# Optimization experiments

Measured on AMD Instinct MI355X. Metric: run time of the kernel, lower is better.

Reference implementation:

```python
import jax, jax.numpy as jnp
import numpy as np

N_USER = 100000
N_ITEM = 150000
N = N_USER + N_ITEM
D = 64            # latdim
NNZ = 1250000     # sparse adjacency nnz
BATCH = 16384     # node_ids batch
NUM_GNN_LAYERS = 2
GD = 16           # gate_dim (mamba d_model)
DSTATE = 8
DCONV = 4
EXPAND = 2
DINNER = GD * EXPAND  # 32
DTRANK = 1            # ceil(GD/16)
TEMP = 0.8            # gate_temp


def setup_inputs() -> dict:
    key = jax.random.key(0)
    ks = jax.random.split(key, 20)
    f32 = jnp.float32
    inp = {}
    inp["user_embedding"] = jax.random.normal(ks[0], (N_USER, D), f32) * 0.02
    inp["item_embedding"] = jax.random.normal(ks[1], (N_ITEM, D), f32) * 0.02
    inp["edge_row"] = jax.random.randint(ks[2], (NNZ,), 0, N, dtype=jnp.int32)
    inp["edge_col"] = jax.random.randint(ks[3], (NNZ,), 0, N, dtype=jnp.int32)
    inp["edge_val"] = jax.random.uniform(ks[4], (NNZ,), f32) * 0.1
    inp["node_ids"] = jax.random.randint(ks[5], (BATCH,), 0, N, dtype=jnp.int32)
    # gate params (torch Linear weight layout: [out, in])
    inp["down_w"] = jax.random.normal(ks[6], (GD, D), f32) * 0.02
    inp["in_proj_w"] = jax.random.normal(ks[7], (2 * DINNER, GD), f32) * 0.05
    inp["conv_w"] = jax.random.normal(ks[8], (DINNER, DCONV), f32) * 0.1
    inp["conv_b"] = jnp.zeros((DINNER,), f32)
    inp["x_proj_w"] = jax.random.normal(ks[9], (DTRANK + 2 * DSTATE, DINNER), f32) * 0.05
    inp["dt_proj_w"] = jax.random.normal(ks[10], (DINNER, DTRANK), f32) * 0.1
    inp["dt_proj_b"] = jax.random.normal(ks[11], (DINNER,), f32) * 0.1
    inp["A_log"] = jnp.log(jnp.broadcast_to(jnp.arange(1, DSTATE + 1, dtype=f32), (DINNER, DSTATE)))
    inp["D_param"] = jnp.ones((DINNER,), f32)
    inp["out_proj_w"] = jax.random.normal(ks[12], (GD, DINNER), f32) * 0.05
    inp["ln_g"] = jnp.ones((GD,), f32)
    inp["ln_b"] = jnp.zeros((GD,), f32)
    inp["to_logit_w"] = jax.random.normal(ks[13], (1, GD), f32) * 0.02
    inp["to_logit_b"] = jnp.zeros((1,), f32)
    return inp


def _mamba(g, in_proj_w, conv_w, conv_b, x_proj_w, dt_proj_w, dt_proj_b, A_log, D_param, out_proj_w):
    # g: [B, L, GD] -- standard Mamba block (selective scan)
    Bsz, L, _ = g.shape
    xz = g @ in_proj_w.T                     # [B,L,2*DINNER]
    x, z = jnp.split(xz, 2, axis=-1)         # each [B,L,DINNER]
    # causal depthwise conv1d along L (padding = DCONV-1, truncated to L)
    xp = jnp.pad(x, ((0, 0), (DCONV - 1, 0), (0, 0)))
    xconv = sum(xp[:, k:k + L, :] * conv_w[:, k] for k in range(DCONV)) + conv_b
    x = jax.nn.silu(xconv)
    dbc = x @ x_proj_w.T                     # [B,L,DTRANK+2*DSTATE]
    dt = dbc[..., :DTRANK]
    Bm = dbc[..., DTRANK:DTRANK + DSTATE]
    Cm = dbc[..., DTRANK + DSTATE:]
    dt = jax.nn.softplus(dt @ dt_proj_w.T + dt_proj_b)   # [B,L,DINNER]
    A = -jnp.exp(A_log)                                   # [DINNER,DSTATE]
    dA = jnp.exp(dt[..., None] * A)                       # [B,L,DINNER,DSTATE]
    dBx = dt[..., None] * Bm[:, :, None, :] * x[..., None]

    def step(h, ins):
        dA_t, dBx_t = ins
        h = dA_t * h + dBx_t
        return h, h

    h0 = jnp.zeros((Bsz, DINNER, DSTATE), x.dtype)
    _, hs = jax.lax.scan(step, h0, (jnp.swapaxes(dA, 0, 1), jnp.swapaxes(dBx, 0, 1)))
    hs = jnp.swapaxes(hs, 0, 1)                           # [B,L,DINNER,DSTATE]
    y = jnp.einsum('blds,bls->bld', hs, Cm) + D_param * x
    y = y * jax.nn.silu(z)
    return y @ out_proj_w.T                               # [B,L,GD]


def reference(user_embedding, item_embedding, edge_val, down_w, in_proj_w, conv_w,
              conv_b, x_proj_w, dt_proj_w, dt_proj_b, A_log, D_param, out_proj_w,
              ln_g, ln_b, to_logit_w, to_logit_b, edge_row, edge_col, node_ids):
    embeds = jnp.concatenate([user_embedding, item_embedding], axis=0)   # [N,D]
    seqs = [embeds[node_ids]]
    for _ in range(NUM_GNN_LAYERS):
        # sparse adjacency aggregation: out[r] += val * embeds[c]
        msg = edge_val[:, None] * embeds[edge_col]                       # [NNZ,D]
        embeds = jax.ops.segment_sum(msg, edge_row, num_segments=N)      # [N,D]
        # F.normalize(p=2, dim=1)
        nrm = jnp.linalg.norm(embeds, axis=1, keepdims=True)
        embeds = embeds / jnp.maximum(nrm, 1e-12)
        seqs.append(embeds[node_ids])
    seq = jnp.stack(seqs, axis=1)                                        # [B,L,D]

    # MambaDepthGating._compute_logits (deg_cond disabled)
    g = seq @ down_w.T                                                   # [B,L,GD]
    y = _mamba(g, in_proj_w, conv_w, conv_b, x_proj_w, dt_proj_w, dt_proj_b,
               A_log, D_param, out_proj_w)
    y = y + g
    mu = y.mean(-1, keepdims=True)
    var = y.var(-1, keepdims=True)
    y = (y - mu) / jnp.sqrt(var + 1e-12) * ln_g + ln_b                   # LN eps=1e-12
    logits = (y @ to_logit_w.T + to_logit_b)[..., 0]                     # [B,L]

    # fuse_from_logits, L=3 > 2 -> softmax path, perturbed=False
    w = jax.nn.softmax(logits / max(TEMP, 1e-6), axis=1)                 # [B,L]
    fused = jnp.sum(seq * w[..., None], axis=1)                          # [B,D]
    return fused
```

## Files before the change

kernel.cpp:

```cpp
#include <hip/hip_runtime.h>
#include <math.h>

#define N_USER 100000
#define N_ITEM 150000
#define NTOT   250000
#define D64    64
#define NNZ    1250000
#define BATCH  16384
#define GD     16
#define DSTATE 8
#define DCONV  4
#define DINNER 32
#define LSEQ   3
#define NBLK1  ((NTOT + 1023) >> 10)

__global__ void mark_nids_kernel(const int* __restrict__ nids,
                                 unsigned char* __restrict__ nidf,
                                 unsigned char* __restrict__ needf) {
    int b = blockIdx.x * 256 + threadIdx.x;
    if (b < BATCH) { int r = nids[b]; nidf[r] = 1; needf[r] = 1; }
}

__global__ void mark_need_kernel(const int* __restrict__ erow,
                                 const int* __restrict__ ecol,
                                 const unsigned char* __restrict__ nidf,
                                 unsigned char* __restrict__ needf) {
    int e = (blockIdx.x * 256 + threadIdx.x) * 4;
    if (e + 4 <= NNZ) {
        int4 r = *(const int4*)(erow + e);
        int4 c = *(const int4*)(ecol + e);
        if (nidf[r.x]) needf[c.x] = 1;
        if (nidf[r.y]) needf[c.y] = 1;
        if (nidf[r.z]) needf[c.z] = 1;
        if (nidf[r.w]) needf[c.w] = 1;
    } else {
        for (; e < NNZ; ++e) if (nidf[erow[e]]) needf[ecol[e]] = 1;
    }
}

__global__ void hist_kernel(const int* __restrict__ erow,
                            const unsigned char* __restrict__ needf,
                            int* __restrict__ cnt) {
    int e = (blockIdx.x * 256 + threadIdx.x) * 4;
    if (e + 4 <= NNZ) {
        int4 r = *(const int4*)(erow + e);
        if (needf[r.x]) atomicAdd(&cnt[r.x], 1);
        if (needf[r.y]) atomicAdd(&cnt[r.y], 1);
        if (needf[r.z]) atomicAdd(&cnt[r.z], 1);
        if (needf[r.w]) atomicAdd(&cnt[r.w], 1);
    } else {
        for (; e < NNZ; ++e) {
            int r = erow[e];
            if (needf[r]) atomicAdd(&cnt[r], 1);
        }
    }
}

__global__ __launch_bounds__(256) void scan1_kernel(const int* __restrict__ cnt,
                                                    const unsigned char* __restrict__ flags,
                                                    int* __restrict__ offs,
                                                    int* __restrict__ fpos,
                                                    int* __restrict__ bsum,
                                                    int* __restrict__ fbsum) {
    __shared__ int lds[256];
    __shared__ int lfs[256];
    int t = threadIdx.x;
    int base = (blockIdx.x << 10) + (t << 2);
    int d0 = (base + 0 < NTOT) ? cnt[base + 0] : 0;
    int d1 = (base + 1 < NTOT) ? cnt[base + 1] : 0;
    int d2 = (base + 2 < NTOT) ? cnt[base + 2] : 0;
    int d3 = (base + 3 < NTOT) ? cnt[base + 3] : 0;
    int f0 = (base + 0 < NTOT) ? (int)flags[base + 0] : 0;
    int f1 = (base + 1 < NTOT) ? (int)flags[base + 1] : 0;
    int f2 = (base + 2 < NTOT) ? (int)flags[base + 2] : 0;
    int f3 = (base + 3 < NTOT) ? (int)flags[base + 3] : 0;
    int s  = d0 + d1 + d2 + d3;
    int fs = f0 + f1 + f2 + f3;
    lds[t] = s; lfs[t] = fs;
    __syncthreads();
    for (int off = 1; off < 256; off <<= 1) {
        int v  = (t >= off) ? lds[t - off] : 0;
        int fv = (t >= off) ? lfs[t - off] : 0;
        __syncthreads();
        lds[t] += v; lfs[t] += fv;
        __syncthreads();
    }
    int excl  = lds[t] - s;
    int fexcl = lfs[t] - fs;
    if (base + 0 < NTOT) { offs[base + 0] = excl;                fpos[base + 0] = fexcl; }
    if (base + 1 < NTOT) { offs[base + 1] = excl + d0;           fpos[base + 1] = fexcl + f0; }
    if (base + 2 < NTOT) { offs[base + 2] = excl + d0 + d1;      fpos[base + 2] = fexcl + f0 + f1; }
    if (base + 3 < NTOT) { offs[base + 3] = excl + d0 + d1 + d2; fpos[base + 3] = fexcl + f0 + f1 + f2; }
    if (t == 255) { bsum[blockIdx.x] = lds[255]; fbsum[blockIdx.x] = lfs[255]; }
}

__global__ __launch_bounds__(256) void scan2_kernel(int* __restrict__ bsum,
                                                    int* __restrict__ fbsum) {
    __shared__ int lds[256];
    __shared__ int lfs[256];
    int t = threadIdx.x;
    int v0 = (t < NBLK1) ? bsum[t] : 0;
    int f0 = (t < NBLK1) ? fbsum[t] : 0;
    lds[t] = v0; lfs[t] = f0;
    __syncthreads();
    for (int off = 1; off < 256; off <<= 1) {
        int v  = (t >= off) ? lds[t - off] : 0;
        int fv = (t >= off) ? lfs[t - off] : 0;
        __syncthreads();
        lds[t] += v; lfs[t] += fv;
        __syncthreads();
    }
    if (t < NBLK1) { bsum[t] = lds[t] - v0; fbsum[t] = lfs[t] - f0; }
}

__global__ void scan3_kernel(int* __restrict__ offs, const int* __restrict__ bsum,
                             const int* __restrict__ cnt,
                             const int* __restrict__ fpos, const int* __restrict__ fbsum,
                             const unsigned char* __restrict__ flags,
                             int* __restrict__ cursor,
                             int* __restrict__ row_list, int* __restrict__ nrows) {
    int i = blockIdx.x * 256 + threadIdx.x;
    if (i >= NTOT) return;
    int v = offs[i] + bsum[i >> 10];
    offs[i] = v;
    cursor[i] = v;
    int fp = fpos[i] + fbsum[i >> 10];
    int fl = flags[i];
    if (fl) row_list[fp] = i;
    if (i == NTOT - 1) {
        offs[NTOT] = v + cnt[i];
        nrows[0] = fp + fl;
    }
}

__global__ void fill_kernel(const int* __restrict__ erow, const int* __restrict__ ecol,
                            const float* __restrict__ eval_,
                            int* __restrict__ cursor,
                            const unsigned char* __restrict__ needf,
                            int2* __restrict__ colval) {
    int e = (blockIdx.x * 256 + threadIdx.x) * 4;
    if (e + 4 <= NNZ) {
        int4   r = *(const int4*)(erow + e);
        int4   c = *(const int4*)(ecol + e);
        float4 v = *(const float4*)(eval_ + e);
        if (needf[r.x]) colval[atomicAdd(&cursor[r.x], 1)] = make_int2(c.x, __float_as_int(v.x));
        if (needf[r.y]) colval[atomicAdd(&cursor[r.y], 1)] = make_int2(c.y, __float_as_int(v.y));
        if (needf[r.z]) colval[atomicAdd(&cursor[r.z], 1)] = make_int2(c.z, __float_as_int(v.z));
        if (needf[r.w]) colval[atomicAdd(&cursor[r.w], 1)] = make_int2(c.w, __float_as_int(v.w));
    } else {
        for (; e < NNZ; ++e) {
            int r = erow[e];
            if (needf[r]) colval[atomicAdd(&cursor[r], 1)] = make_int2(ecol[e], __float_as_int(eval_[e]));
        }
    }
}

__global__ __launch_bounds__(256) void layer1_kernel(const float* __restrict__ user,
                                                     const float* __restrict__ item,
                                                     const int*  __restrict__ nrows,
                                                     const int*  __restrict__ row_list,
                                                     const int*  __restrict__ offs,
                                                     const int2* __restrict__ colval,
                                                     float* __restrict__ dst) {
    const float4* user4 = (const float4*)user;
    const float4* item4 = (const float4*)item;

    int gid    = (blockIdx.x << 4) + (threadIdx.x >> 4);
    int lane16 = threadIdx.x & 15;
    if (gid >= nrows[0]) return;
    int row = row_list[gid];
    int o0 = offs[row], o1 = offs[row + 1];

    float4 acc = make_float4(0.f, 0.f, 0.f, 0.f);
    int i = o0;
    for (; i + 4 <= o1; i += 4) {
        int2 cv0 = colval[i], cv1 = colval[i + 1], cv2 = colval[i + 2], cv3 = colval[i + 3];
        const float4* s0 = (cv0.x < N_USER) ? user4 + (size_t)cv0.x * 16
                                            : item4 + (size_t)(cv0.x - N_USER) * 16;
        const float4* s1 = (cv1.x < N_USER) ? user4 + (size_t)cv1.x * 16
                                            : item4 + (size_t)(cv1.x - N_USER) * 16;
        const float4* s2 = (cv2.x < N_USER) ? user4 + (size_t)cv2.x * 16
                                            : item4 + (size_t)(cv2.x - N_USER) * 16;
        const float4* s3 = (cv3.x < N_USER) ? user4 + (size_t)cv3.x * 16
                                            : item4 + (size_t)(cv3.x - N_USER) * 16;
        float4 v0 = s0[lane16], v1 = s1[lane16], v2 = s2[lane16], v3 = s3[lane16];
        float w0 = __int_as_float(cv0.y), w1 = __int_as_float(cv1.y);
        float w2 = __int_as_float(cv2.y), w3 = __int_as_float(cv3.y);
        acc.x = fmaf(w3, v3.x, fmaf(w2, v2.x, fmaf(w1, v1.x, fmaf(w0, v0.x, acc.x))));
        acc.y = fmaf(w3, v3.y, fmaf(w2, v2.y, fmaf(w1, v1.y, fmaf(w0, v0.y, acc.y))));
        acc.z = fmaf(w3, v3.z, fmaf(w2, v2.z, fmaf(w1, v1.z, fmaf(w0, v0.z, acc.z))));
        acc.w = fmaf(w3, v3.w, fmaf(w2, v2.w, fmaf(w1, v1.w, fmaf(w0, v0.w, acc.w))));
    }
    for (; i < o1; ++i) {
        int2 cv = colval[i];
        const float4* s0 = (cv.x < N_USER) ? user4 + (size_t)cv.x * 16
                                           : item4 + (size_t)(cv.x - N_USER) * 16;
        float4 v = s0[lane16];
        float w = __int_as_float(cv.y);
        acc.x = fmaf(w, v.x, acc.x);
        acc.y = fmaf(w, v.y, acc.y);
        acc.z = fmaf(w, v.z, acc.z);
        acc.w = fmaf(w, v.w, acc.w);
    }

    float s = fmaf(acc.x, acc.x, fmaf(acc.y, acc.y, fmaf(acc.z, acc.z, acc.w * acc.w)));
    #pragma unroll
    for (int m = 8; m >= 1; m >>= 1) s += __shfl_xor(s, m, 64);
    float scale = 1.f / fmaxf(sqrtf(s), 1e-12f);
    float4 r;
    r.x = acc.x * scale; r.y = acc.y * scale; r.z = acc.z * scale; r.w = acc.w * scale;
    ((float4*)dst)[(size_t)row * 16 + lane16] = r;
}

__global__ __launch_bounds__(256) void final_kernel(
    const int*   __restrict__ nids,
    const float* __restrict__ user,      const float* __restrict__ item,
    const float* __restrict__ embA,
    const int*   __restrict__ offs,      const int2* __restrict__ colval,
    const float* __restrict__ down_w,    const float* __restrict__ in_proj_w,
    const float* __restrict__ conv_w,    const float* __restrict__ conv_b,
    const float* __restrict__ x_proj_w,  const float* __restrict__ dt_proj_w,
    const float* __restrict__ dt_proj_b, const float* __restrict__ A_log,
    const float* __restrict__ D_param,   const float* __restrict__ out_proj_w,
    const float* __restrict__ ln_g,      const float* __restrict__ ln_b,
    const float* __restrict__ to_logit_w,const float* __restrict__ to_logit_b,
    float* __restrict__ out) {

    __shared__ float4 s_rows4[16 * 49];
    __shared__ float  s_downT[D64 * GD];
    __shared__ float  s_ipxT[GD * DINNER];
    __shared__ float  s_ipzT[GD * DINNER];
    __shared__ float  s_xpT[DINNER * 17];
    __shared__ float  s_opT[DINNER * GD];
    __shared__ float  s_AT[DSTATE * DINNER];
    __shared__ float4 s_cw4[DINNER];
    __shared__ float  s_cb[DINNER], s_dtw[DINNER], s_dtb[DINNER], s_Dp[DINNER];
    __shared__ float  s_lng[GD], s_lnb[GD], s_lw[GD];
    __shared__ float  s_lb;
    __shared__ float  s_g[16 * 49];
    __shared__ float  s_xs[16 * 98];
    __shared__ float  s_dbc[16 * 49];

    int t = threadIdx.x;
    int wave = t >> 6, lane = t & 63;
    int grp = lane >> 4, lane16 = lane & 15;
    int eb = wave * 4 + grp;
    int b  = blockIdx.x * 16 + eb;
    int nid = nids[b];

    {
        const float4* p0 = (const float4*)((nid < N_USER) ? user + (size_t)nid * D64
                                                          : item + (size_t)(nid - N_USER) * D64);
        const float4* p1 = (const float4*)(embA + (size_t)nid * D64);
        s_rows4[eb * 49 + 0 * 16 + lane16] = p0[lane16];
        s_rows4[eb * 49 + 1 * 16 + lane16] = p1[lane16];

        const float4* src4 = (const float4*)embA;
        int o0 = offs[nid], o1 = offs[nid + 1];
        float4 acc = make_float4(0.f, 0.f, 0.f, 0.f);
        int i = o0;
        for (; i + 4 <= o1; i += 4) {
            int2 cv0 = colval[i], cv1 = colval[i + 1], cv2 = colval[i + 2], cv3 = colval[i + 3];
            float4 v0 = src4[(size_t)cv0.x * 16 + lane16];
            float4 v1 = src4[(size_t)cv1.x * 16 + lane16];
            float4 v2 = src4[(size_t)cv2.x * 16 + lane16];
            float4 v3 = src4[(size_t)cv3.x * 16 + lane16];
            float w0 = __int_as_float(cv0.y), w1 = __int_as_float(cv1.y);
            float w2 = __int_as_float(cv2.y), w3 = __int_as_float(cv3.y);
            acc.x = fmaf(w3, v3.x, fmaf(w2, v2.x, fmaf(w1, v1.x, fmaf(w0, v0.x, acc.x))));
            acc.y = fmaf(w3, v3.y, fmaf(w2, v2.y, fmaf(w1, v1.y, fmaf(w0, v0.y, acc.y))));
            acc.z = fmaf(w3, v3.z, fmaf(w2, v2.z, fmaf(w1, v1.z, fmaf(w0, v0.z, acc.z))));
            acc.w = fmaf(w3, v3.w, fmaf(w2, v2.w, fmaf(w1, v1.w, fmaf(w0, v0.w, acc.w))));
        }
        for (; i < o1; ++i) {
            int2 cv = colval[i];
            float4 v = src4[(size_t)cv.x * 16 + lane16];
            float w = __int_as_float(cv.y);
            acc.x = fmaf(w, v.x, acc.x);
            acc.y = fmaf(w, v.y, acc.y);
            acc.z = fmaf(w, v.z, acc.z);
            acc.w = fmaf(w, v.w, acc.w);
        }
        float s = fmaf(acc.x, acc.x, fmaf(acc.y, acc.y, fmaf(acc.z, acc.z, acc.w * acc.w)));
        #pragma unroll
        for (int m = 8; m >= 1; m >>= 1) s += __shfl_xor(s, m, 64);
        float scale = 1.f / fmaxf(sqrtf(s), 1e-12f);
        float4 r;
        r.x = acc.x * scale; r.y = acc.y * scale; r.z = acc.z * scale; r.w = acc.w * scale;
        s_rows4[eb * 49 + 2 * 16 + lane16] = r;
    }

    for (int i = t; i < D64 * GD; i += 256) {
        int j = i & 15, d = i >> 4;
        s_downT[i] = down_w[j * D64 + d];
    }
    for (int i = t; i < GD * DINNER; i += 256) {
        int d = i & 31, j = i >> 5;
        s_ipxT[i] = in_proj_w[d * GD + j];
        s_ipzT[i] = in_proj_w[(d + DINNER) * GD + j];
    }
    for (int i = t; i < DINNER * 17; i += 256) {
        int d = i / 17, r = i % 17;
        s_xpT[i] = x_proj_w[r * DINNER + d];
    }
    for (int i = t; i < DINNER * GD; i += 256) {
        int j = i & 15, d = i >> 4;
        s_opT[i] = out_proj_w[j * DINNER + d];
    }
    for (int i = t; i < DSTATE * DINNER; i += 256) {
        int d = i & 31, s = i >> 5;
        s_AT[i] = -expf(A_log[d * DSTATE + s]);
    }
    if (t < DINNER) {
        s_cw4[t] = ((const float4*)conv_w)[t];
        s_cb[t] = conv_b[t]; s_dtw[t] = dt_proj_w[t];
        s_dtb[t] = dt_proj_b[t]; s_Dp[t] = D_param[t];
    }
    if (t < GD) { s_lng[t] = ln_g[t]; s_lnb[t] = ln_b[t]; s_lw[t] = to_logit_w[t]; }
    if (t == 0) s_lb = to_logit_b[0];
    __syncthreads();

    const float* rows = (const float*)s_rows4 + eb * 196;

    {
        float a0 = 0.f, a1 = 0.f, a2 = 0.f;
        #pragma unroll
        for (int d = 0; d < D64; ++d) {
            float w = s_downT[d * GD + lane16];
            a0 = fmaf(rows[d], w, a0);
            a1 = fmaf(rows[64 + d], w, a1);
            a2 = fmaf(rows[128 + d], w, a2);
        }
        s_g[eb * 49 + 0 * GD + lane16] = a0;
        s_g[eb * 49 + 1 * GD + lane16] = a1;
        s_g[eb * 49 + 2 * GD + lane16] = a2;
    }
    __syncthreads();

    const float* ge = s_g + eb * 49;

    float xsr[2][LSEQ];
    #pragma unroll
    for (int c = 0; c < 2; ++c) {
        int d = lane16 + 16 * c;
        float xl0 = 0.f, xl1 = 0.f, xl2 = 0.f;
        #pragma unroll
        for (int j = 0; j < GD; ++j) {
            float w = s_ipxT[j * DINNER + d];
            xl0 = fmaf(ge[j], w, xl0);
            xl1 = fmaf(ge[GD + j], w, xl1);
            xl2 = fmaf(ge[2 * GD + j], w, xl2);
        }
        float4 cw = s_cw4[d]; float cb = s_cb[d];
        float a0 = fmaf(xl0, cw.w, cb);
        float a1 = fmaf(xl1, cw.w, fmaf(xl0, cw.z, cb));
        float a2 = fmaf(xl2, cw.w, fmaf(xl1, cw.z, fmaf(xl0, cw.y, cb)));
        xsr[c][0] = a0 / (1.f + __expf(-a0));
        xsr[c][1] = a1 / (1.f + __expf(-a1));
        xsr[c][2] = a2 / (1.f + __expf(-a2));
        #pragma unroll
        for (int l = 0; l < LSEQ; ++l) s_xs[eb * 98 + l * DINNER + d] = xsr[c][l];
    }
    __syncthreads();

    {
        const float* xse = s_xs + eb * 98;
        int nr = (lane16 == 0) ? 2 : 1;
        for (int it = 0; it < nr; ++it) {
            int r = (it == 0) ? lane16 : 16;
            float a0 = 0.f, a1 = 0.f, a2 = 0.f;
            #pragma unroll
            for (int d = 0; d < DINNER; ++d) {
                float w = s_xpT[d * 17 + r];
                a0 = fmaf(xse[d], w, a0);
                a1 = fmaf(xse[DINNER + d], w, a1);
                a2 = fmaf(xse[2 * DINNER + d], w, a2);
            }
            s_dbc[eb * 49 + 0 * 17 + r] = a0;
            s_dbc[eb * 49 + 1 * 17 + r] = a1;
            s_dbc[eb * 49 + 2 * 17 + r] = a2;
        }
    }
    __syncthreads();

    {
        const float* dbce = s_dbc + eb * 49;
        float h[2][DSTATE];
        #pragma unroll
        for (int c = 0; c < 2; ++c)
            #pragma unroll
            for (int s = 0; s < DSTATE; ++s) h[c][s] = 0.f;
        #pragma unroll
        for (int l = 0; l < LSEQ; ++l) {
            float dtr = dbce[l * 17];
            float Bm[DSTATE], Cm[DSTATE];
            #pragma unroll
            for (int s = 0; s < DSTATE; ++s) {
                Bm[s] = dbce[l * 17 + 1 + s];
                Cm[s] = dbce[l * 17 + 9 + s];
            }
            #pragma unroll
            for (int c = 0; c < 2; ++c) {
                int d = lane16 + 16 * c;
                float pre = fmaf(dtr, s_dtw[d], s_dtb[d]);
                float dt  = (pre > 20.f) ? pre : __logf(1.f + __expf(pre));
                float xv  = xsr[c][l];
                float dtx = dt * xv;
                float acc = 0.f;
                #pragma unroll
                for (int s = 0; s < DSTATE; ++s) {
                    float dA = __expf(dt * s_AT[s * DINNER + d]);
                    h[c][s] = fmaf(dA, h[c][s], dtx * Bm[s]);
                    acc = fmaf(h[c][s], Cm[s], acc);
                }
                float y = fmaf(s_Dp[d], xv, acc);
                float zv = 0.f;
                #pragma unroll
                for (int j = 0; j < GD; ++j)
                    zv = fmaf(ge[l * GD + j], s_ipzT[j * DINNER + d], zv);
                float ys = y * (zv / (1.f + __expf(-zv)));
                s_xs[eb * 98 + l * DINNER + d] = ys;
            }
        }
    }
    __syncthreads();

    float lg[LSEQ];
    {
        const float* yse = s_xs + eb * 98;
        #pragma unroll
        for (int l = 0; l < LSEQ; ++l) {
            float a = 0.f;
            #pragma unroll
            for (int d = 0; d < DINNER; ++d)
                a = fmaf(yse[l * DINNER + d], s_opT[d * GD + lane16], a);
            float v = a + ge[l * GD + lane16];
            float sm = v, sq = v * v;
            #pragma unroll
            for (int m = 1; m <= 8; m <<= 1) {
                sm += __shfl_xor(sm, m, 64);
                sq += __shfl_xor(sq, m, 64);
            }
            float mu  = sm * (1.f / GD);
            float var = fmaxf(sq * (1.f / GD) - mu * mu, 0.f);
            float inv = rsqrtf(var + 1e-12f);
            float lo = fmaf(fmaf((v - mu) * inv, s_lng[lane16], s_lnb[lane16]),
                            s_lw[lane16], 0.f);
            #pragma unroll
            for (int m = 1; m <= 8; m <<= 1) lo += __shfl_xor(lo, m, 64);
            lg[l] = (lo + s_lb) * 1.25f;
        }
    }

    {
        float mx = fmaxf(lg[0], fmaxf(lg[1], lg[2]));
        float e0 = __expf(lg[0] - mx), e1 = __expf(lg[1] - mx), e2 = __expf(lg[2] - mx);
        float inv = 1.f / (e0 + e1 + e2);
        float w0 = e0 * inv, w1 = e1 * inv, w2 = e2 * inv;
        float4 r0 = s_rows4[eb * 49 + 0 * 16 + lane16];
        float4 r1 = s_rows4[eb * 49 + 1 * 16 + lane16];
        float4 r2 = s_rows4[eb * 49 + 2 * 16 + lane16];
        float4 r;
        r.x = w0 * r0.x + w1 * r1.x + w2 * r2.x;
        r.y = w0 * r0.y + w1 * r1.y + w2 * r2.y;
        r.z = w0 * r0.z + w1 * r1.z + w2 * r2.z;
        r.w = w0 * r0.w + w1 * r1.w + w2 * r2.w;
        ((float4*)out)[(size_t)b * 16 + lane16] = r;
    }
}

extern "C" void kernel_launch(void* const* d_in, const int* in_sizes, int n_in,
                              void* d_out, int out_size, void* d_ws, size_t ws_size,
                              hipStream_t stream) {
    const float* user      = (const float*)d_in[0];
    const float* item      = (const float*)d_in[1];
    const int*   erow      = (const int*)  d_in[2];
    const int*   ecol      = (const int*)  d_in[3];
    const float* eval_     = (const float*)d_in[4];
    const int*   nids      = (const int*)  d_in[5];
    const float* down_w    = (const float*)d_in[6];
    const float* in_proj_w = (const float*)d_in[7];
    const float* conv_w    = (const float*)d_in[8];
    const float* conv_b    = (const float*)d_in[9];
    const float* x_proj_w  = (const float*)d_in[10];
    const float* dt_proj_w = (const float*)d_in[11];
    const float* dt_proj_b = (const float*)d_in[12];
    const float* A_log     = (const float*)d_in[13];
    const float* D_param   = (const float*)d_in[14];
    const float* out_projw = (const float*)d_in[15];
    const float* ln_g      = (const float*)d_in[16];
    const float* ln_b      = (const float*)d_in[17];
    const float* to_lw     = (const float*)d_in[18];
    const float* to_lb     = (const float*)d_in[19];
    float* out = (float*)d_out;

    char* base = (char*)d_ws;
    float* embA = (float*)base;
    char* c = base + 64000000;
    int* cnt   = (int*)c;
    unsigned char* nidf  = (unsigned char*)(c + 1000000);
    unsigned char* needf = (unsigned char*)(c + 1250000);
    size_t zbytes = 1500000;
    c += 1500032;
    int* nrows    = (int*)c;  c += 64;
    int* row_list = (int*)c;  c += (size_t)NTOT * 4;
    int* fpos     = (int*)c;  c += (size_t)NTOT * 4;
    int* cursor   = (int*)c;  c += (size_t)NTOT * 4;
    int* offs     = (int*)c;  c += (size_t)(NTOT + 1) * 4 + 60;
    int* bsum     = (int*)c;  c += 1024;
    int* fbsum    = (int*)c;  c += 1024;
    int2* colval  = (int2*)c;

    hipMemsetAsync((void*)cnt, 0, zbytes, stream);

    mark_nids_kernel<<<(BATCH + 255) / 256, 256, 0, stream>>>(nids, nidf, needf);
    mark_need_kernel<<<(NNZ / 4 + 255) / 256, 256, 0, stream>>>(erow, ecol, nidf, needf);

    hist_kernel<<<(NNZ / 4 + 255) / 256, 256, 0, stream>>>(erow, needf, cnt);
    scan1_kernel<<<NBLK1, 256, 0, stream>>>(cnt, needf, offs, fpos, bsum, fbsum);
    scan2_kernel<<<1, 256, 0, stream>>>(bsum, fbsum);
    scan3_kernel<<<(NTOT + 255) / 256, 256, 0, stream>>>(offs, bsum, cnt, fpos, fbsum,
                                                         needf, cursor, row_list, nrows);
    fill_kernel<<<(NNZ / 4 + 255) / 256, 256, 0, stream>>>(erow, ecol, eval_, cursor,
                                                           needf, colval);

    layer1_kernel<<<(NTOT + 15) / 16, 256, 0, stream>>>(user, item, nrows, row_list, offs, colval, embA);

    final_kernel<<<BATCH / 16, 256, 0, stream>>>(nids, user, item, embA, offs, colval,
                                                 down_w, in_proj_w, conv_w, conv_b,
                                                 x_proj_w, dt_proj_w, dt_proj_b, A_log,
                                                 D_param, out_projw, ln_g, ln_b, to_lw, to_lb, out);
}
```

Baseline: 247.7 us.

## Fuse three-pass scan into single-pass decoupled look-back scan with packed row info

Replaces the scan1/scan2/scan3 kernel sequence with one kernel that does a decoupled look-back over per-block partials to get global prefixes for both the degree counts and the compacted row flags. It writes offsets, cursors and a packed int4 per active row (row, start, end), so layer1 reads one record instead of an indirect row_list lookup plus two offs loads. This removes two kernel launches and the intermediate fpos, bsum and fbsum arrays. In exchange it adds serial spin-waiting on earlier blocks (about 245 of them), which depends on those blocks being scheduled, and a larger rowinfo buffer.

```diff
diff --git a/kernel.cpp b/kernel.cpp
--- a/kernel.cpp
+++ b/kernel.cpp
@@ -56,16 +56,22 @@
     }
 }
 
-__global__ __launch_bounds__(256) void scan1_kernel(const int* __restrict__ cnt,
-                                                    const unsigned char* __restrict__ flags,
-                                                    int* __restrict__ offs,
-                                                    int* __restrict__ fpos,
-                                                    int* __restrict__ bsum,
-                                                    int* __restrict__ fbsum) {
+__device__ __forceinline__ unsigned long long pack_part(unsigned long long flag,
+                                                        unsigned long long c,
+                                                        unsigned long long f) {
+    return (flag << 62) | (c << 32) | f;
+}
+
+__global__ __launch_bounds__(256) void scan_fused_kernel(
+        const int* __restrict__ cnt, const unsigned char* __restrict__ flags,
+        int* __restrict__ offs, int* __restrict__ cursor,
+        int4* __restrict__ rowinfo, int* __restrict__ nrows,
+        unsigned long long* __restrict__ partials) {
     __shared__ int lds[256];
     __shared__ int lfs[256];
-    int t = threadIdx.x;
-    int base = (blockIdx.x << 10) + (t << 2);
+    __shared__ int s_base[2];
+    int t = threadIdx.x, blk = blockIdx.x;
+    int base = (blk << 10) + (t << 2);
     int d0 = (base + 0 < NTOT) ? cnt[base + 0] : 0;
     int d1 = (base + 1 < NTOT) ? cnt[base + 1] : 0;
     int d2 = (base + 2 < NTOT) ? cnt[base + 2] : 0;
@@ -85,51 +91,57 @@
         lds[t] += v; lfs[t] += fv;
         __syncthreads();
     }
-    int excl  = lds[t] - s;
-    int fexcl = lfs[t] - fs;
-    if (base + 0 < NTOT) { offs[base + 0] = excl;                fpos[base + 0] = fexcl; }
-    if (base + 1 < NTOT) { offs[base + 1] = excl + d0;           fpos[base + 1] = fexcl + f0; }
-    if (base + 2 < NTOT) { offs[base + 2] = excl + d0 + d1;      fpos[base + 2] = fexcl + f0 + f1; }
-    if (base + 3 < NTOT) { offs[base + 3] = excl + d0 + d1 + d2; fpos[base + 3] = fexcl + f0 + f1 + f2; }
-    if (t == 255) { bsum[blockIdx.x] = lds[255]; fbsum[blockIdx.x] = lfs[255]; }
-}
-
-__global__ __launch_bounds__(256) void scan2_kernel(int* __restrict__ bsum,
-                                                    int* __restrict__ fbsum) {
-    __shared__ int lds[256];
-    __shared__ int lfs[256];
-    int t = threadIdx.x;
-    int v0 = (t < NBLK1) ? bsum[t] : 0;
-    int f0 = (t < NBLK1) ? fbsum[t] : 0;
-    lds[t] = v0; lfs[t] = f0;
-    __syncthreads();
-    for (int off = 1; off < 256; off <<= 1) {
-        int v  = (t >= off) ? lds[t - off] : 0;
-        int fv = (t >= off) ? lfs[t - off] : 0;
-        __syncthreads();
-        lds[t] += v; lfs[t] += fv;
-        __syncthreads();
-    }
-    if (t < NBLK1) { bsum[t] = lds[t] - v0; fbsum[t] = lfs[t] - f0; }
-}
-
-__global__ void scan3_kernel(int* __restrict__ offs, const int* __restrict__ bsum,
-                             const int* __restrict__ cnt,
-                             const int* __restrict__ fpos, const int* __restrict__ fbsum,
-                             const unsigned char* __restrict__ flags,
-                             int* __restrict__ cursor,
-                             int* __restrict__ row_list, int* __restrict__ nrows) {
-    int i = blockIdx.x * 256 + threadIdx.x;
-    if (i >= NTOT) return;
-    int v = offs[i] + bsum[i >> 10];
-    offs[i] = v;
-    cursor[i] = v;
-    int fp = fpos[i] + fbsum[i >> 10];
-    int fl = flags[i];
-    if (fl) row_list[fp] = i;
-    if (i == NTOT - 1) {
-        offs[NTOT] = v + cnt[i];
-        nrows[0] = fp + fl;
+    int totC = lds[255], totF = lfs[255];
+
+    if (t == 0) {
+        if (blk == 0) {
+            __hip_atomic_store(&partials[0], pack_part(2ull, (unsigned long long)totC,
+                                                       (unsigned long long)totF),
+                               __ATOMIC_RELEASE, __HIP_MEMORY_SCOPE_AGENT);
+            s_base[0] = 0; s_base[1] = 0;
+        } else {
+            __hip_atomic_store(&partials[blk], pack_part(1ull, (unsigned long long)totC,
+                                                         (unsigned long long)totF),
+                               __ATOMIC_RELEASE, __HIP_MEMORY_SCOPE_AGENT);
+            int accC = 0, accF = 0;
+            for (int j = blk - 1; j >= 0; --j) {
+                unsigned long long v;
+                do {
+                    v = __hip_atomic_load(&partials[j], __ATOMIC_ACQUIRE,
+                                          __HIP_MEMORY_SCOPE_AGENT);
+                } while ((v >> 62) == 0ull);
+                accC += (int)((v >> 32) & 0x3FFFFFFFull);
+                accF += (int)(v & 0xFFFFFFFFull);
+                if ((v >> 62) == 2ull) break;
+            }
+            s_base[0] = accC; s_base[1] = accF;
+            __hip_atomic_store(&partials[blk],
+                               pack_part(2ull, (unsigned long long)(accC + totC),
+                                         (unsigned long long)(accF + totF)),
+                               __ATOMIC_RELEASE, __HIP_MEMORY_SCOPE_AGENT);
+        }
+    }
+    __syncthreads();
+    int baseC = s_base[0], baseF = s_base[1];
+
+    int exclC = baseC + lds[t] - s;
+    int exclF = baseF + lfs[t] - fs;
+    int offv[4] = { exclC, exclC + d0, exclC + d0 + d1, exclC + d0 + d1 + d2 };
+    int fpv[4]  = { exclF, exclF + f0, exclF + f0 + f1, exclF + f0 + f1 + f2 };
+    int dv[4]   = { d0, d1, d2, d3 };
+    int fv2[4]  = { f0, f1, f2, f3 };
+    #pragma unroll
+    for (int k = 0; k < 4; ++k) {
+        int idx = base + k;
+        if (idx < NTOT) {
+            offs[idx] = offv[k];
+            cursor[idx] = offv[k];
+            if (fv2[k]) rowinfo[fpv[k]] = make_int4(idx, offv[k], offv[k] + dv[k], 0);
+            if (idx == NTOT - 1) {
+                offs[NTOT] = offv[k] + dv[k];
+                nrows[0] = fpv[k] + fv2[k];
+            }
+        }
     }
 }
 
@@ -158,8 +170,7 @@
 __global__ __launch_bounds__(256) void layer1_kernel(const float* __restrict__ user,
                                                      const float* __restrict__ item,
                                                      const int*  __restrict__ nrows,
-                                                     const int*  __restrict__ row_list,
-                                                     const int*  __restrict__ offs,
+                                                     const int4* __restrict__ rowinfo,
                                                      const int2* __restrict__ colval,
                                                      float* __restrict__ dst) {
     const float4* user4 = (const float4*)user;
@@ -168,8 +179,8 @@
     int gid    = (blockIdx.x << 4) + (threadIdx.x >> 4);
     int lane16 = threadIdx.x & 15;
     if (gid >= nrows[0]) return;
-    int row = row_list[gid];
-    int o0 = offs[row], o1 = offs[row + 1];
+    int4 ri = rowinfo[gid];
+    int row = ri.x, o0 = ri.y, o1 = ri.z;
 
     float4 acc = make_float4(0.f, 0.f, 0.f, 0.f);
     int i = o0;
@@ -500,15 +511,13 @@
     int* cnt   = (int*)c;
     unsigned char* nidf  = (unsigned char*)(c + 1000000);
     unsigned char* needf = (unsigned char*)(c + 1250000);
-    size_t zbytes = 1500000;
-    c += 1500032;
+    unsigned long long* partials = (unsigned long long*)(c + 1500000);
+    size_t zbytes = 1502048;
+    c += 1502048;
     int* nrows    = (int*)c;  c += 64;
-    int* row_list = (int*)c;  c += (size_t)NTOT * 4;
-    int* fpos     = (int*)c;  c += (size_t)NTOT * 4;
     int* cursor   = (int*)c;  c += (size_t)NTOT * 4;
     int* offs     = (int*)c;  c += (size_t)(NTOT + 1) * 4 + 60;
-    int* bsum     = (int*)c;  c += 1024;
-    int* fbsum    = (int*)c;  c += 1024;
+    int4* rowinfo = (int4*)c; c += (size_t)NTOT * 16;
     int2* colval  = (int2*)c;
 
     hipMemsetAsync((void*)cnt, 0, zbytes, stream);
@@ -517,14 +526,12 @@
     mark_need_kernel<<<(NNZ / 4 + 255) / 256, 256, 0, stream>>>(erow, ecol, nidf, needf);
 
     hist_kernel<<<(NNZ / 4 + 255) / 256, 256, 0, stream>>>(erow, needf, cnt);
-    scan1_kernel<<<NBLK1, 256, 0, stream>>>(cnt, needf, offs, fpos, bsum, fbsum);
-    scan2_kernel<<<1, 256, 0, stream>>>(bsum, fbsum);
-    scan3_kernel<<<(NTOT + 255) / 256, 256, 0, stream>>>(offs, bsum, cnt, fpos, fbsum,
-                                                         needf, cursor, row_list, nrows);
+    scan_fused_kernel<<<NBLK1, 256, 0, stream>>>(cnt, needf, offs, cursor,
+                                                 rowinfo, nrows, partials);
     fill_kernel<<<(NNZ / 4 + 255) / 256, 256, 0, stream>>>(erow, ecol, eval_, cursor,
                                                            needf, colval);
 
-    layer1_kernel<<<(NTOT + 15) / 16, 256, 0, stream>>>(user, item, nrows, row_list, offs, colval, embA);
+    layer1_kernel<<<(NTOT + 15) / 16, 256, 0, stream>>>(user, item, nrows, rowinfo, colval, embA);
 
     final_kernel<<<BATCH / 16, 256, 0, stream>>>(nids, user, item, embA, offs, colval,
                                                  down_w, in_proj_w, conv_w, conv_b,
```

Measured after the change: 298.8 us. 1.21x slower.
